# Kernel tuning notes

Measured on AMD Instinct MI355X. Metric: run time of the kernel, lower is better.

Reference implementation:

```python
import jax, jax.numpy as jnp
import numpy as np

N = 768
C = 256  # in_features == out_features (required by Linear(in_features+3, 1))

def _leaky(x):
    return jnp.where(x >= 0, x, 0.2 * x)

def setup_inputs() -> dict:
    key = jax.random.key(0)
    ks = jax.random.split(key, 10)
    features = jax.random.normal(ks[0], (N, C), dtype=jnp.float32)
    coordinates = jax.random.normal(ks[1], (N, 3), dtype=jnp.float32)
    adj = jax.random.uniform(ks[2], (N, N), dtype=jnp.float32)  # unused by forward, kept for signature fidelity
    # Learned params
    FC = jax.random.normal(ks[3], (C, C), dtype=jnp.float32) * (1.414 / jnp.sqrt(C))
    # Conv1d(2,1,kernel=1): weight [out=1, in=2, k=1] -> 2 scalars + bias
    fc_w = jax.random.normal(ks[4], (2,), dtype=jnp.float32) * 0.5
    fc_b = jax.random.normal(ks[5], (1,), dtype=jnp.float32) * 0.1
    sc_w = jax.random.normal(ks[6], (2,), dtype=jnp.float32) * 0.5
    sc_b = jax.random.normal(ks[7], (1,), dtype=jnp.float32) * 0.1
    # Linear(C+3, 1)
    lin_w = jax.random.normal(ks[8], (C + 3,), dtype=jnp.float32) * (1.0 / jnp.sqrt(C + 3))
    lin_b = jax.random.normal(ks[9], (1,), dtype=jnp.float32) * 0.1
    return {"features": features, "coordinates": coordinates, "adj": adj,
            "FC": FC, "fc_w": fc_w, "fc_b": fc_b, "sc_w": sc_w, "sc_b": sc_b,
            "lin_w": lin_w, "lin_b": lin_b}

def reference(features, coordinates, adj, FC, fc_w, fc_b, sc_w, sc_b, lin_w, lin_b):
    n = features.shape[0]
    f_input = features @ FC  # [N, C]
    # torch's repeat(1,N).view + repeat(N,1) builds pairs (i, j); the 1x1 Conv1d over
    # the 2 stacked channels is exactly w0*x_i + w1*x_j + b, then LeakyReLU(0.2).
    f_map = _leaky(fc_w[0] * f_input[:, None, :] + fc_w[1] * f_input[None, :, :] + fc_b[0])  # [N,N,C]
    s_map = _leaky(sc_w[0] * coordinates[:, None, :] + sc_w[1] * coordinates[None, :, :] + sc_b[0])  # [N,N,3]
    # Linear(C+3, 1) on cat([f_map, s_map], -1), then LeakyReLU -> [N, N]
    scores = _leaky(jnp.einsum('ijc,c->ij', f_map, lin_w[:f_input.shape[1]])
                    + jnp.einsum('ijk,k->ij', s_map, lin_w[f_input.shape[1]:])
                    + lin_b[0])
    attention = jax.nn.softmax(scores, axis=1)  # row softmax (dim=1)
    h_prime = attention @ f_input  # [N, C]
    return jax.nn.elu(h_prime)  # concat=True path
```

## Files before the change

kernel.cpp:

```cpp
#include <hip/hip_runtime.h>
#include <math.h>

#define NN 768
#define CC 256
#define TI 3

__device__ __forceinline__ float leaky(float x) { return x >= 0.0f ? x : 0.2f * x; }

__device__ __forceinline__ float waveMax(float v) {
    #pragma unroll
    for (int o = 32; o > 0; o >>= 1) v = fmaxf(v, __shfl_xor(v, o, 64));
    return v;
}
__device__ __forceinline__ float waveSum(float v) {
    #pragma unroll
    for (int o = 32; o > 0; o >>= 1) v += __shfl_xor(v, o, 64);
    return v;
}

__global__ __launch_bounds__(768) void k_prep(
    const float* __restrict__ features,
    const float* __restrict__ FC,
    const float* __restrict__ fc_w,
    const float* __restrict__ fc_b,
    const float* __restrict__ lin_w,
    float* __restrict__ f,
    float* __restrict__ g,
    float* __restrict__ D0,
    float* __restrict__ D1)
{
    __shared__ float sA[TI * CC];
    __shared__ float sredD[12], sredW[12];

    const int t  = threadIdx.x;
    const int r  = t >> 8;
    const int c  = t & 255;
    const int i0 = blockIdx.x * TI;

    sA[r * CC + c] = features[(i0 + r) * CC + c];
    __syncthreads();

    float a = 0.f;
    const float* fcp = FC + c;
    const float* ap  = sA + r * CC;
    #pragma unroll 8
    for (int k = 0; k < CC; ++k)
        a = fmaf(ap[k], fcp[k * CC], a);

    const float w1 = fc_w[1], b = fc_b[0];
    f[(i0 + r) * CC + c] = a;
    g[c * NN + i0 + r]   = fmaf(w1, a, b);

    const float lw = lin_w[c];
    float dv = waveSum(lw * a);
    float wv = waveSum(lw);
    const int wid = t >> 6;
    if ((t & 63) == 0) { sredD[wid] = dv; sredW[wid] = wv; }
    __syncthreads();
    if (t < TI) {
        float D = sredD[t*4] + sredD[t*4+1] + sredD[t*4+2] + sredD[t*4+3];
        float W = sredW[t*4] + sredW[t*4+1] + sredW[t*4+2] + sredW[t*4+3];
        D0[i0 + t] = fc_w[0] * D;
        D1[i0 + t] = fmaf(w1, D, b * W);
    }
}

__global__ __launch_bounds__(768) void k_attn(
    const float* __restrict__ f,
    const float* __restrict__ g,
    const float* __restrict__ D0,
    const float* __restrict__ D1,
    const float* __restrict__ coords,
    const float* __restrict__ fc_w,
    const float* __restrict__ sc_w,
    const float* __restrict__ sc_b,
    const float* __restrict__ lin_w,
    const float* __restrict__ lin_b,
    float* __restrict__ out)
{
    __shared__ float4 spack[CC];
    __shared__ float4 pp[NN];
    __shared__ float  spart[TI][TI][CC];
    __shared__ float  sredm[12][TI];
    __shared__ float  sreds[12][TI];

    const int t    = threadIdx.x;
    const int i0   = blockIdx.x * TI;
    const int wid  = t >> 6;
    const int lane = t & 63;

    const float w0 = fc_w[0];
    if (t < CC) {
        spack[t] = make_float4(w0 * f[(i0+0)*CC + t],
                               w0 * f[(i0+1)*CC + t],
                               w0 * f[(i0+2)*CC + t],
                               0.4f * lin_w[t]);
    }

    const float lw30 = lin_w[CC+0], lw31 = lin_w[CC+1], lw32 = lin_w[CC+2];
    const float sw0 = sc_w[0], sw1 = sc_w[1], sb = sc_b[0], lb = lin_b[0];

    float ax[TI][3];
    #pragma unroll
    for (int r = 0; r < TI; ++r) {
        ax[r][0] = sw0 * coords[(i0+r)*3+0];
        ax[r][1] = sw0 * coords[(i0+r)*3+1];
        ax[r][2] = sw0 * coords[(i0+r)*3+2];
    }
    float bse[TI];
    #pragma unroll
    for (int r = 0; r < TI; ++r) bse[r] = fmaf(0.6f, D0[i0+r], lb);
    const float d1j = D1[t];
    __syncthreads();

    float s0 = 0.f, s1 = 0.f, s2 = 0.f;
    const float* gp = g + t;
    #pragma unroll 8
    for (int c = 0; c < CC; ++c) {
        float gj = gp[c * NN];
        float4 u = spack[c];
        s0 = fmaf(u.w, fabsf(u.x + gj), s0);
        s1 = fmaf(u.w, fabsf(u.y + gj), s1);
        s2 = fmaf(u.w, fabsf(u.z + gj), s2);
    }

    float c0 = fmaf(sw1, coords[t*3+0], sb);
    float c1 = fmaf(sw1, coords[t*3+1], sb);
    float c2 = fmaf(sw1, coords[t*3+2], sb);
    float sacc[TI] = {s0, s1, s2};
    float scv[TI];
    #pragma unroll
    for (int r = 0; r < TI; ++r) {
        float sd = lw30*leaky(ax[r][0]+c0) + lw31*leaky(ax[r][1]+c1) + lw32*leaky(ax[r][2]+c2);
        scv[r] = leaky(sacc[r] + sd + fmaf(0.6f, d1j, bse[r]));
    }

    #pragma unroll
    for (int r = 0; r < TI; ++r) {
        float v = waveMax(scv[r]);
        if (lane == 0) sredm[wid][r] = v;
    }
    __syncthreads();
    float m[TI];
    #pragma unroll
    for (int r = 0; r < TI; ++r) {
        float v = sredm[0][r];
        #pragma unroll
        for (int w = 1; w < 12; ++w) v = fmaxf(v, sredm[w][r]);
        m[r] = v;
    }
    float e0 = __expf(scv[0] - m[0]);
    float e1 = __expf(scv[1] - m[1]);
    float e2 = __expf(scv[2] - m[2]);
    pp[t] = make_float4(e0, e1, e2, 0.f);
    float es[TI] = {e0, e1, e2};
    #pragma unroll
    for (int r = 0; r < TI; ++r) {
        float v = waveSum(es[r]);
        if (lane == 0) sreds[wid][r] = v;
    }
    __syncthreads();
    float inv[TI];
    #pragma unroll
    for (int r = 0; r < TI; ++r) {
        float v = 0.f;
        #pragma unroll
        for (int w = 0; w < 12; ++w) v += sreds[w][r];
        inv[r] = 1.0f / v;
    }

    const int q = t >> 8;
    const int c = t & 255;
    float h0 = 0.f, h1 = 0.f, h2 = 0.f;
    const float* fp = f + (q * 256) * CC + c;
    const float4* pq = pp + q * 256;
    #pragma unroll 8
    for (int jj = 0; jj < 256; ++jj) {
        float fv = fp[jj * CC];
        float4 p = pq[jj];
        h0 = fmaf(p.x, fv, h0);
        h1 = fmaf(p.y, fv, h1);
        h2 = fmaf(p.z, fv, h2);
    }
    spart[q][0][c] = h0;
    spart[q][1][c] = h1;
    spart[q][2][c] = h2;
    __syncthreads();
    if (t < CC) {
        #pragma unroll
        for (int r = 0; r < TI; ++r) {
            float h = spart[0][r][t] + spart[1][r][t] + spart[2][r][t];
            float v = h * inv[r];
            out[(i0 + r) * CC + t] = (v > 0.f) ? v : (__expf(v) - 1.0f);
        }
    }
}

extern "C" void kernel_launch(void* const* d_in, const int* in_sizes, int n_in,
                              void* d_out, int out_size, void* d_ws, size_t ws_size,
                              hipStream_t stream) {
    const float* features = (const float*)d_in[0];
    const float* coords   = (const float*)d_in[1];
    const float* FC       = (const float*)d_in[3];
    const float* fc_w     = (const float*)d_in[4];
    const float* fc_b     = (const float*)d_in[5];
    const float* sc_w     = (const float*)d_in[6];
    const float* sc_b     = (const float*)d_in[7];
    const float* lin_w    = (const float*)d_in[8];
    const float* lin_b    = (const float*)d_in[9];
    float* out = (float*)d_out;

    float* f  = (float*)d_ws;
    float* g  = f + NN*CC;
    float* D0 = g + CC*NN;
    float* D1 = D0 + NN;

    k_prep<<<NN/TI, TI*256, 0, stream>>>(features, FC, fc_w, fc_b, lin_w, f, g, D0, D1);
    k_attn<<<NN/TI, TI*256, 0, stream>>>(f, g, D0, D1, coords, fc_w, sc_w, sc_b, lin_w, lin_b, out);
}
```

Before: 119.7 us.

## Split attention over column chunks with flash-style partial softmax combine

The attention kernel now handles 12 rows per block over a 192-column chunk, with 4 chunks per row tile. Each block writes a partial row max, partial sum and partial h, and a new combine kernel merges them with log-sum-exp rescaling before applying ELU. This reuses each g and f load across 12 rows instead of 3 and keeps the grid size the same, aiming to cut global memory traffic in the score and aggregation loops. The cost is an extra kernel launch and a round trip of the partial h buffer through global memory.

```diff
diff --git a/kernel.cpp b/kernel.cpp
--- a/kernel.cpp
+++ b/kernel.cpp
@@ -4,6 +4,9 @@
 #define NN 768
 #define CC 256
 #define TI 3
+#define RT 12
+#define JC 192
+#define NJC 4
 
 __device__ __forceinline__ float leaky(float x) { return x >= 0.0f ? x : 0.2f * x; }
 
@@ -76,124 +79,138 @@
     const float* __restrict__ sc_b,
     const float* __restrict__ lin_w,
     const float* __restrict__ lin_b,
+    float* __restrict__ hp,
+    float* __restrict__ Mp,
+    float* __restrict__ Lp)
+{
+    __shared__ float4 su4[4 * CC];
+    __shared__ float  pe[RT * JC];
+    __shared__ float  sredm[12][3];
+    __shared__ float  sreds[12][3];
+
+    const int t  = threadIdx.x;
+    const int it = blockIdx.x >> 2;
+    const int jc = blockIdx.x & 3;
+    const int i0 = it * RT;
+    const int jb = jc * JC;
+    const int q  = t / JC;
+    const int jj = t - q * JC;
+    const int j  = jb + jj;
+    const int wid  = t >> 6;
+    const int lane = t & 63;
+
+    if (t < CC) {
+        const float w0  = fc_w[0];
+        const float wl4 = 0.4f * lin_w[t];
+        #pragma unroll
+        for (int qq = 0; qq < 4; ++qq)
+            su4[qq * CC + t] = make_float4(w0 * f[(i0 + 3*qq + 0)*CC + t],
+                                           w0 * f[(i0 + 3*qq + 1)*CC + t],
+                                           w0 * f[(i0 + 3*qq + 2)*CC + t],
+                                           wl4);
+    }
+    __syncthreads();
+
+    float a0 = 0.f, a1 = 0.f, a2 = 0.f;
+    const float*  gp  = g + j;
+    const float4* sup = su4 + q * CC;
+    #pragma unroll 8
+    for (int c = 0; c < CC; ++c) {
+        float  gj = gp[c * NN];
+        float4 u  = sup[c];
+        a0 = fmaf(u.w, fabsf(u.x + gj), a0);
+        a1 = fmaf(u.w, fabsf(u.y + gj), a1);
+        a2 = fmaf(u.w, fabsf(u.z + gj), a2);
+    }
+
+    const float sw0 = sc_w[0], sw1 = sc_w[1], sb = sc_b[0], lb = lin_b[0];
+    const float lw30 = lin_w[CC], lw31 = lin_w[CC+1], lw32 = lin_w[CC+2];
+    const float cj0 = fmaf(sw1, coords[j*3+0], sb);
+    const float cj1 = fmaf(sw1, coords[j*3+1], sb);
+    const float cj2 = fmaf(sw1, coords[j*3+2], sb);
+    const float d1  = D1[j];
+    float accs[3] = {a0, a1, a2};
+    float scv[3];
+    #pragma unroll
+    for (int rr = 0; rr < 3; ++rr) {
+        const int i = i0 + 3*q + rr;
+        float sd = lw30 * leaky(fmaf(sw0, coords[i*3+0], cj0))
+                 + lw31 * leaky(fmaf(sw0, coords[i*3+1], cj1))
+                 + lw32 * leaky(fmaf(sw0, coords[i*3+2], cj2));
+        scv[rr] = leaky(accs[rr] + sd + 0.6f * (D0[i] + d1) + lb);
+    }
+
+    #pragma unroll
+    for (int rr = 0; rr < 3; ++rr) {
+        float v = waveMax(scv[rr]);
+        if (lane == 0) sredm[wid][rr] = v;
+    }
+    __syncthreads();
+    float m[3];
+    #pragma unroll
+    for (int rr = 0; rr < 3; ++rr)
+        m[rr] = fmaxf(fmaxf(sredm[3*q][rr], sredm[3*q+1][rr]), sredm[3*q+2][rr]);
+
+    float e[3];
+    #pragma unroll
+    for (int rr = 0; rr < 3; ++rr) {
+        e[rr] = __expf(scv[rr] - m[rr]);
+        pe[(3*q + rr) * JC + jj] = e[rr];
+        float v = waveSum(e[rr]);
+        if (lane == 0) sreds[wid][rr] = v;
+    }
+    __syncthreads();
+    if (jj == 0) {
+        #pragma unroll
+        for (int rr = 0; rr < 3; ++rr) {
+            float l = sreds[3*q][rr] + sreds[3*q+1][rr] + sreds[3*q+2][rr];
+            Mp[(i0 + 3*q + rr) * NJC + jc] = m[rr];
+            Lp[(i0 + 3*q + rr) * NJC + jc] = l;
+        }
+    }
+
+    const int rg = t >> 8;
+    const int c  = t & 255;
+    float h0 = 0.f, h1 = 0.f, h2 = 0.f, h3 = 0.f;
+    const float* fp  = f + jb * CC + c;
+    const float* pep = pe + (4 * rg) * JC;
+    #pragma unroll 4
+    for (int jx = 0; jx < JC; ++jx) {
+        float fv = fp[jx * CC];
+        h0 = fmaf(pep[jx],          fv, h0);
+        h1 = fmaf(pep[JC + jx],     fv, h1);
+        h2 = fmaf(pep[2*JC + jx],   fv, h2);
+        h3 = fmaf(pep[3*JC + jx],   fv, h3);
+    }
+    float* hpp = hp + ((size_t)jc * NN + i0 + 4*rg) * CC + c;
+    hpp[0]      = h0;
+    hpp[CC]     = h1;
+    hpp[2*CC]   = h2;
+    hpp[3*CC]   = h3;
+}
+
+__global__ __launch_bounds__(256) void k_comb(
+    const float* __restrict__ hp,
+    const float* __restrict__ Mp,
+    const float* __restrict__ Lp,
     float* __restrict__ out)
 {
-    __shared__ float4 spack[CC];
-    __shared__ float4 pp[NN];
-    __shared__ float  spart[TI][TI][CC];
-    __shared__ float  sredm[12][TI];
-    __shared__ float  sreds[12][TI];
-
-    const int t    = threadIdx.x;
-    const int i0   = blockIdx.x * TI;
-    const int wid  = t >> 6;
-    const int lane = t & 63;
-
-    const float w0 = fc_w[0];
-    if (t < CC) {
-        spack[t] = make_float4(w0 * f[(i0+0)*CC + t],
-                               w0 * f[(i0+1)*CC + t],
-                               w0 * f[(i0+2)*CC + t],
-                               0.4f * lin_w[t]);
-    }
-
-    const float lw30 = lin_w[CC+0], lw31 = lin_w[CC+1], lw32 = lin_w[CC+2];
-    const float sw0 = sc_w[0], sw1 = sc_w[1], sb = sc_b[0], lb = lin_b[0];
-
-    float ax[TI][3];
-    #pragma unroll
-    for (int r = 0; r < TI; ++r) {
-        ax[r][0] = sw0 * coords[(i0+r)*3+0];
-        ax[r][1] = sw0 * coords[(i0+r)*3+1];
-        ax[r][2] = sw0 * coords[(i0+r)*3+2];
-    }
-    float bse[TI];
-    #pragma unroll
-    for (int r = 0; r < TI; ++r) bse[r] = fmaf(0.6f, D0[i0+r], lb);
-    const float d1j = D1[t];
-    __syncthreads();
-
-    float s0 = 0.f, s1 = 0.f, s2 = 0.f;
-    const float* gp = g + t;
-    #pragma unroll 8
-    for (int c = 0; c < CC; ++c) {
-        float gj = gp[c * NN];
-        float4 u = spack[c];
-        s0 = fmaf(u.w, fabsf(u.x + gj), s0);
-        s1 = fmaf(u.w, fabsf(u.y + gj), s1);
-        s2 = fmaf(u.w, fabsf(u.z + gj), s2);
-    }
-
-    float c0 = fmaf(sw1, coords[t*3+0], sb);
-    float c1 = fmaf(sw1, coords[t*3+1], sb);
-    float c2 = fmaf(sw1, coords[t*3+2], sb);
-    float sacc[TI] = {s0, s1, s2};
-    float scv[TI];
-    #pragma unroll
-    for (int r = 0; r < TI; ++r) {
-        float sd = lw30*leaky(ax[r][0]+c0) + lw31*leaky(ax[r][1]+c1) + lw32*leaky(ax[r][2]+c2);
-        scv[r] = leaky(sacc[r] + sd + fmaf(0.6f, d1j, bse[r]));
-    }
-
-    #pragma unroll
-    for (int r = 0; r < TI; ++r) {
-        float v = waveMax(scv[r]);
-        if (lane == 0) sredm[wid][r] = v;
-    }
-    __syncthreads();
-    float m[TI];
-    #pragma unroll
-    for (int r = 0; r < TI; ++r) {
-        float v = sredm[0][r];
-        #pragma unroll
-        for (int w = 1; w < 12; ++w) v = fmaxf(v, sredm[w][r]);
-        m[r] = v;
-    }
-    float e0 = __expf(scv[0] - m[0]);
-    float e1 = __expf(scv[1] - m[1]);
-    float e2 = __expf(scv[2] - m[2]);
-    pp[t] = make_float4(e0, e1, e2, 0.f);
-    float es[TI] = {e0, e1, e2};
-    #pragma unroll
-    for (int r = 0; r < TI; ++r) {
-        float v = waveSum(es[r]);
-        if (lane == 0) sreds[wid][r] = v;
-    }
-    __syncthreads();
-    float inv[TI];
-    #pragma unroll
-    for (int r = 0; r < TI; ++r) {
-        float v = 0.f;
-        #pragma unroll
-        for (int w = 0; w < 12; ++w) v += sreds[w][r];
-        inv[r] = 1.0f / v;
-    }
-
-    const int q = t >> 8;
-    const int c = t & 255;
-    float h0 = 0.f, h1 = 0.f, h2 = 0.f;
-    const float* fp = f + (q * 256) * CC + c;
-    const float4* pq = pp + q * 256;
-    #pragma unroll 8
-    for (int jj = 0; jj < 256; ++jj) {
-        float fv = fp[jj * CC];
-        float4 p = pq[jj];
-        h0 = fmaf(p.x, fv, h0);
-        h1 = fmaf(p.y, fv, h1);
-        h2 = fmaf(p.z, fv, h2);
-    }
-    spart[q][0][c] = h0;
-    spart[q][1][c] = h1;
-    spart[q][2][c] = h2;
-    __syncthreads();
-    if (t < CC) {
-        #pragma unroll
-        for (int r = 0; r < TI; ++r) {
-            float h = spart[0][r][t] + spart[1][r][t] + spart[2][r][t];
-            float v = h * inv[r];
-            out[(i0 + r) * CC + t] = (v > 0.f) ? v : (__expf(v) - 1.0f);
-        }
-    }
+    const int t = threadIdx.x;
+    const int i = blockIdx.x;
+
+    float m0 = Mp[i*NJC+0], m1 = Mp[i*NJC+1], m2 = Mp[i*NJC+2], m3 = Mp[i*NJC+3];
+    float M  = fmaxf(fmaxf(m0, m1), fmaxf(m2, m3));
+    float w0 = __expf(m0 - M), w1 = __expf(m1 - M);
+    float w2 = __expf(m2 - M), w3 = __expf(m3 - M);
+    float den = w0*Lp[i*NJC+0] + w1*Lp[i*NJC+1] + w2*Lp[i*NJC+2] + w3*Lp[i*NJC+3];
+    float inv = 1.0f / den;
+
+    float num = w0 * hp[((size_t)0*NN + i)*CC + t]
+              + w1 * hp[((size_t)1*NN + i)*CC + t]
+              + w2 * hp[((size_t)2*NN + i)*CC + t]
+              + w3 * hp[((size_t)3*NN + i)*CC + t];
+    float v = num * inv;
+    out[i*CC + t] = (v > 0.f) ? v : (__expf(v) - 1.0f);
 }
 
 extern "C" void kernel_launch(void* const* d_in, const int* in_sizes, int n_in,
@@ -211,10 +228,15 @@
     float* out = (float*)d_out;
 
     float* f  = (float*)d_ws;
-    float* g  = f + NN*CC;
-    float* D0 = g + CC*NN;
+    float* g  = f  + NN*CC;
+    float* D0 = g  + CC*NN;
     float* D1 = D0 + NN;
-
-    k_prep<<<NN/TI, TI*256, 0, stream>>>(features, FC, fc_w, fc_b, lin_w, f, g, D0, D1);
-    k_attn<<<NN/TI, TI*256, 0, stream>>>(f, g, D0, D1, coords, fc_w, sc_w, sc_b, lin_w, lin_b, out);
-}
+    float* Mp = D1 + NN;
+    float* Lp = Mp + NN*NJC;
+    float* hp = Lp + NN*NJC;
+
+    k_prep<<<NN/TI, 768, 0, stream>>>(features, FC, fc_w, fc_b, lin_w, f, g, D0, D1);
+    k_attn<<<(NN/RT)*NJC, 768, 0, stream>>>(f, g, D0, D1, coords, fc_w, sc_w, sc_b,
+                                            lin_w, lin_b, hp, Mp, Lp);
+    k_comb<<<NN, 256, 0, stream>>>(hp, Mp, Lp, out);
+}
```

Result: no change. 118.7 us (-0.9%).
